# Kernel optimization log

Measured on AMD Instinct MI355X. Metric: run time of the kernel, lower is better.

The kernel has to match this reference:

```python
import jax, jax.numpy as jnp
import numpy as np


def setup_inputs() -> dict:
    key = jax.random.key(0)
    k1, k2, k3, k4 = jax.random.split(key, 4)
    B, C, H, W = 32, 1, 512, 512
    return {
        "cancer_logits": jax.random.normal(k1, (B, C, H, W), dtype=jnp.float32),
        "label": jax.random.uniform(k2, (B,), dtype=jnp.float32),
        "prostate_mask": jax.random.uniform(k3, (B, 1, H, W), dtype=jnp.float32),
        "needle_mask": jax.random.uniform(k4, (B, 1, H, W), dtype=jnp.float32),
    }


def reference(cancer_logits, label, prostate_mask, needle_mask):
    # Valid region = prostate AND needle masks thresholded at 0.5.
    mask = (prostate_mask > 0.5) & (needle_mask > 0.5)          # [B,1,H,W] bool
    x = cancer_logits                                            # [B,1,H,W]
    y = label[:, None, None, None]                               # broadcast per-core label to pixels
    # Numerically-stable BCE with logits: max(x,0) - x*y + log(1+exp(-|x|))
    bce = jnp.maximum(x, 0.0) - x * y + jnp.log1p(jnp.exp(-jnp.abs(x)))
    m = mask.astype(x.dtype)
    # Mean over the selected (valid) elements == sum(bce*m)/count, same as
    # F.binary_cross_entropy_with_logits on the gathered logits/labels.
    count = jnp.maximum(jnp.sum(m), 1.0)
    return jnp.sum(bce * m) / count
```

## Files before the change

### kernel.cpp

```cpp
#include <hip/hip_runtime.h>
#include <math.h>

constexpr int HW_SIZE = 512 * 512;
constexpr int NB      = 32;
constexpr int N       = NB * HW_SIZE;
constexpr int N4      = N / 4;
constexpr int BLOCK   = 256;
constexpr int K       = 2;
constexpr int GRID1   = N4 / (BLOCK * K);
constexpr int NWAVES  = GRID1 * (BLOCK / 64);

__global__ __launch_bounds__(BLOCK) void loss_partial(
    const float4* __restrict__ x4,
    const float*  __restrict__ label,
    const float4* __restrict__ pm4,
    const float4* __restrict__ nm4,
    float2* __restrict__ partials) {
  const int i = blockIdx.x * (BLOCK * K) + threadIdx.x;
  const float y = label[blockIdx.x >> 7];

  const float4 xv0 = x4[i];
  const float4 xv1 = x4[i + BLOCK];
  const float4 pv0 = pm4[i];
  const float4 pv1 = pm4[i + BLOCK];
  const float4 nv0 = nm4[i];
  const float4 nv1 = nm4[i + BLOCK];
  __builtin_amdgcn_sched_barrier(0);

  float s_bce = 0.0f;
  float s_cnt = 0.0f;
  const float xs[8] = {xv0.x, xv0.y, xv0.z, xv0.w, xv1.x, xv1.y, xv1.z, xv1.w};
  const float ps[8] = {pv0.x, pv0.y, pv0.z, pv0.w, pv1.x, pv1.y, pv1.z, pv1.w};
  const float ns[8] = {nv0.x, nv0.y, nv0.z, nv0.w, nv1.x, nv1.y, nv1.z, nv1.w};
#pragma unroll
  for (int j = 0; j < 8; ++j) {
    const float m  = (fminf(ps[j], ns[j]) > 0.5f) ? 1.0f : 0.0f;
    const float xi = xs[j];
    const float sp  = __logf(1.0f + __expf(-fabsf(xi)));
    const float bce = fmaxf(xi, 0.0f) - xi * y + sp;
    s_bce = fmaf(bce, m, s_bce);
    s_cnt += m;
  }

#pragma unroll
  for (int off = 32; off > 0; off >>= 1) {
    s_bce += __shfl_down(s_bce, off);
    s_cnt += __shfl_down(s_cnt, off);
  }
  const int lane = threadIdx.x & 63;
  const int wave = threadIdx.x >> 6;
  if (lane == 0) {
    partials[blockIdx.x * (BLOCK / 64) + wave] = make_float2(s_bce, s_cnt);
  }
}

__global__ __launch_bounds__(1024) void loss_finalize(
    const float2* __restrict__ partials, float* __restrict__ out) {
  float s_bce = 0.0f;
  float s_cnt = 0.0f;
  const float4* p4 = (const float4*)partials;
#pragma unroll
  for (int k = 0; k < NWAVES / 2 / 1024; ++k) {
    const float4 v = p4[k * 1024 + threadIdx.x];
    s_bce += v.x + v.z;
    s_cnt += v.y + v.w;
  }
#pragma unroll
  for (int off = 32; off > 0; off >>= 1) {
    s_bce += __shfl_down(s_bce, off);
    s_cnt += __shfl_down(s_cnt, off);
  }
  __shared__ float sb[16];
  __shared__ float sc[16];
  const int lane = threadIdx.x & 63;
  const int wave = threadIdx.x >> 6;
  if (lane == 0) {
    sb[wave] = s_bce;
    sc[wave] = s_cnt;
  }
  __syncthreads();
  if (threadIdx.x == 0) {
    float tb = 0.0f, tc = 0.0f;
#pragma unroll
    for (int w = 0; w < 16; ++w) { tb += sb[w]; tc += sc[w]; }
    out[0] = tb / fmaxf(tc, 1.0f);
  }
}

extern "C" void kernel_launch(void* const* d_in, const int* in_sizes, int n_in,
                              void* d_out, int out_size, void* d_ws, size_t ws_size,
                              hipStream_t stream) {
  const float4* x4    = (const float4*)d_in[0];
  const float*  label = (const float*)d_in[1];
  const float4* pm4   = (const float4*)d_in[2];
  const float4* nm4   = (const float4*)d_in[3];
  float2* partials = (float2*)d_ws;
  float*  out      = (float*)d_out;

  loss_partial<<<GRID1, BLOCK, 0, stream>>>(x4, label, pm4, nm4, partials);
  loss_finalize<<<1, 1024, 0, stream>>>(partials, out);
}
```

Before: 118.6 us.

## Fuse partial and final reduction via last-block atomic counter

Merges the two-kernel reduction into one kernel. Each block reduces its waves in shared memory, publishes one packed partial with a release store, and bumps a global counter; the last block to arrive sums all partials and writes the result. This drops the second kernel launch and its dependency gap, but adds a memset launch for the counter and one device-scope atomic per block.

```diff
diff --git a/kernel.cpp b/kernel.cpp
--- a/kernel.cpp
+++ b/kernel.cpp
@@ -7,15 +7,28 @@
 constexpr int N4      = N / 4;
 constexpr int BLOCK   = 256;
 constexpr int K       = 2;
-constexpr int GRID1   = N4 / (BLOCK * K);
-constexpr int NWAVES  = GRID1 * (BLOCK / 64);
+constexpr int GRID    = N4 / (BLOCK * K);
 
-__global__ __launch_bounds__(BLOCK) void loss_partial(
+static __device__ inline unsigned long long pack2(float a, float b) {
+  float2 f = make_float2(a, b);
+  unsigned long long u;
+  __builtin_memcpy(&u, &f, 8);
+  return u;
+}
+static __device__ inline float2 unpack2(unsigned long long u) {
+  float2 f;
+  __builtin_memcpy(&f, &u, 8);
+  return f;
+}
+
+__global__ __launch_bounds__(BLOCK) void loss_fused(
     const float4* __restrict__ x4,
     const float*  __restrict__ label,
     const float4* __restrict__ pm4,
     const float4* __restrict__ nm4,
-    float2* __restrict__ partials) {
+    unsigned long long* __restrict__ partials,
+    unsigned int* __restrict__ counter,
+    float* __restrict__ out) {
   const int i = blockIdx.x * (BLOCK * K) + threadIdx.x;
   const float y = label[blockIdx.x >> 7];
 
@@ -47,31 +60,10 @@
     s_bce += __shfl_down(s_bce, off);
     s_cnt += __shfl_down(s_cnt, off);
   }
-  const int lane = threadIdx.x & 63;
-  const int wave = threadIdx.x >> 6;
-  if (lane == 0) {
-    partials[blockIdx.x * (BLOCK / 64) + wave] = make_float2(s_bce, s_cnt);
-  }
-}
 
-__global__ __launch_bounds__(1024) void loss_finalize(
-    const float2* __restrict__ partials, float* __restrict__ out) {
-  float s_bce = 0.0f;
-  float s_cnt = 0.0f;
-  const float4* p4 = (const float4*)partials;
-#pragma unroll
-  for (int k = 0; k < NWAVES / 2 / 1024; ++k) {
-    const float4 v = p4[k * 1024 + threadIdx.x];
-    s_bce += v.x + v.z;
-    s_cnt += v.y + v.w;
-  }
-#pragma unroll
-  for (int off = 32; off > 0; off >>= 1) {
-    s_bce += __shfl_down(s_bce, off);
-    s_cnt += __shfl_down(s_cnt, off);
-  }
-  __shared__ float sb[16];
-  __shared__ float sc[16];
+  __shared__ float sb[4];
+  __shared__ float sc[4];
+  __shared__ bool  is_last;
   const int lane = threadIdx.x & 63;
   const int wave = threadIdx.x >> 6;
   if (lane == 0) {
@@ -80,10 +72,43 @@
   }
   __syncthreads();
   if (threadIdx.x == 0) {
+    const float tb = sb[0] + sb[1] + sb[2] + sb[3];
+    const float tc = sc[0] + sc[1] + sc[2] + sc[3];
+    __hip_atomic_store(&partials[blockIdx.x], pack2(tb, tc),
+                       __ATOMIC_RELEASE, __HIP_MEMORY_SCOPE_AGENT);
+    const unsigned done = __hip_atomic_fetch_add(
+        counter, 1u, __ATOMIC_ACQ_REL, __HIP_MEMORY_SCOPE_AGENT);
+    is_last = (done == GRID - 1);
+  }
+  __syncthreads();
+
+  if (is_last) {
     float tb = 0.0f, tc = 0.0f;
 #pragma unroll
-    for (int w = 0; w < 16; ++w) { tb += sb[w]; tc += sc[w]; }
-    out[0] = tb / fmaxf(tc, 1.0f);
+    for (int k = 0; k < GRID / BLOCK; ++k) {
+      const unsigned long long u = __hip_atomic_load(
+          &partials[k * BLOCK + threadIdx.x],
+          __ATOMIC_RELAXED, __HIP_MEMORY_SCOPE_AGENT);
+      const float2 f = unpack2(u);
+      tb += f.x;
+      tc += f.y;
+    }
+#pragma unroll
+    for (int off = 32; off > 0; off >>= 1) {
+      tb += __shfl_down(tb, off);
+      tc += __shfl_down(tc, off);
+    }
+    __syncthreads();
+    if (lane == 0) {
+      sb[wave] = tb;
+      sc[wave] = tc;
+    }
+    __syncthreads();
+    if (threadIdx.x == 0) {
+      const float fb = sb[0] + sb[1] + sb[2] + sb[3];
+      const float fc = sc[0] + sc[1] + sc[2] + sc[3];
+      out[0] = fb / fmaxf(fc, 1.0f);
+    }
   }
 }
 
@@ -94,9 +119,11 @@
   const float*  label = (const float*)d_in[1];
   const float4* pm4   = (const float4*)d_in[2];
   const float4* nm4   = (const float4*)d_in[3];
-  float2* partials = (float2*)d_ws;
-  float*  out      = (float*)d_out;
+  unsigned long long* partials = (unsigned long long*)d_ws;
+  unsigned int*       counter  = (unsigned int*)(partials + GRID);
+  float*              out      = (float*)d_out;
 
-  loss_partial<<<GRID1, BLOCK, 0, stream>>>(x4, label, pm4, nm4, partials);
-  loss_finalize<<<1, 1024, 0, stream>>>(partials, out);
+  hipMemsetAsync(counter, 0, sizeof(unsigned int), stream);
+  loss_fused<<<GRID, BLOCK, 0, stream>>>(x4, label, pm4, nm4,
+                                         partials, counter, out);
 }
```

Result: slower. 400.3 us (+237.6%).
